# Kernel tuning notes

Hardware: AMD Instinct MI355X
Metric: run time of the kernel (lower is better)

## Reference

```python
import jax, jax.numpy as jnp
import numpy as np

N = 100000
E = 1600000
F_DIM = 128
HEADS = 8
C = F_DIM // HEADS  # 16
NEG_SLOPE = 0.2
EPS = 1e-5


def setup_inputs() -> dict:
    key = jax.random.key(0)
    ks = jax.random.split(key, 12)
    s = 1.0 / np.sqrt(F_DIM)
    x = jax.random.normal(ks[0], (N, F_DIM), dtype=jnp.float32)
    edge_index = jax.random.randint(ks[1], (2, E), 0, N, dtype=jnp.int32)
    edge_attr = jax.random.uniform(ks[2], (E, 1), dtype=jnp.float32)
    W_src = jax.random.normal(ks[3], (F_DIM, HEADS * C), dtype=jnp.float32) * s
    b_src = jnp.zeros((HEADS * C,), dtype=jnp.float32)
    W_dst = jax.random.normal(ks[4], (F_DIM, HEADS * C), dtype=jnp.float32) * s
    b_dst = jnp.zeros((HEADS * C,), dtype=jnp.float32)
    W_edge = jax.random.normal(ks[5], (1, HEADS * C), dtype=jnp.float32)
    att = jax.random.normal(ks[6], (HEADS, C), dtype=jnp.float32) * (1.0 / np.sqrt(C))
    bias = jnp.zeros((HEADS * C,), dtype=jnp.float32)
    gamma = jnp.ones((F_DIM,), dtype=jnp.float32)
    beta = jnp.zeros((F_DIM,), dtype=jnp.float32)
    return {"x": x, "edge_index": edge_index, "edge_attr": edge_attr,
            "W_src": W_src, "b_src": b_src, "W_dst": W_dst, "b_dst": b_dst,
            "W_edge": W_edge, "att": att, "bias": bias,
            "gamma": gamma, "beta": beta}


def _gatv2_block(x, edge_index, edge_attr, W_src, b_src, W_dst, b_dst, W_edge, att, bias, gamma, beta):
    src = edge_index[0]  # message sources j
    dst = edge_index[1]  # message targets i
    # linear projections, per-head view [N, H, C]
    x_src = (x @ W_src + b_src).reshape(N, HEADS, C)
    x_dst = (x @ W_dst + b_dst).reshape(N, HEADS, C)
    e_emb = (edge_attr @ W_edge).reshape(E, HEADS, C)
    # GATv2 edge scores: a^T LeakyReLU(x_i + x_j + e_ij)
    msg_src = x_src[src]                                   # [E, H, C]
    h = jax.nn.leaky_relu(msg_src + x_dst[dst] + e_emb, NEG_SLOPE)
    logits = jnp.einsum('ehc,hc->eh', h, att)              # [E, H]
    # segment softmax over incoming edges of each target node
    m = jax.ops.segment_max(logits, dst, num_segments=N)   # [N, H]
    m = jnp.where(jnp.isfinite(m), m, 0.0)
    ex = jnp.exp(logits - m[dst])
    denom = jax.ops.segment_sum(ex, dst, num_segments=N)   # [N, H]
    alpha = ex / (denom[dst] + 1e-16)                      # [E, H]
    # weighted aggregation (dropout disabled: eval mode)
    out = jax.ops.segment_sum(alpha[:, :, None] * msg_src, dst, num_segments=N)
    out = out.reshape(N, HEADS * C) + bias
    # LayerNorm over feature dim
    mu = jnp.mean(out, axis=-1, keepdims=True)
    var = jnp.var(out, axis=-1, keepdims=True)
    out = (out - mu) * jax.lax.rsqrt(var + EPS) * gamma + beta
    out = jax.nn.elu(out)
    return out + x  # residual


def reference(x, edge_index, edge_attr, W_src, b_src, W_dst, b_dst, W_edge, att, bias, gamma, beta):
    return _gatv2_block(x, edge_index, edge_attr, W_src, b_src, W_dst, b_dst, W_edge, att, bias, gamma, beta)
```

## Files before the change

### kernel.cpp

```cpp
#include <hip/hip_runtime.h>
#include <hip/hip_fp16.h>

#define NN 100000
#define EE 1600000
#define CAP 64
#define NEG_SLOPE 0.2f
#define NEG_INF (-1e30f)

#define NPART 196
#define PSHIFT 9
#define CAPP 10240
#define EPB 4096
#define P1_BLOCKS 391

struct alignas(8) H4 { __half2 a, b; };
struct alignas(16) H8 { __half2 a, b, c, d; };

using f16x8 = __attribute__((ext_vector_type(8))) _Float16;
using f32x4 = __attribute__((ext_vector_type(4))) float;

__global__ __launch_bounds__(512) void partition_kernel(
    const int* __restrict__ ei, const float* __restrict__ eattr,
    int* __restrict__ partCount, uint2* __restrict__ partBuf) {
  __shared__ int hist[NPART];
  __shared__ int base[NPART];
  for (int i = threadIdx.x; i < NPART; i += 512) hist[i] = 0;
  __syncthreads();
  const int e0 = blockIdx.x * EPB;
  int p[8], rank[8];
  uint2 rec[8];
#pragma unroll
  for (int j = 0; j < 8; ++j) {
    const int e = e0 + j * 512 + threadIdx.x;
    if (e < EE) {
      const int dst = ei[EE + e];
      const int src = ei[e];
      const unsigned q = (unsigned)__float2uint_rn(eattr[e] * 32767.0f);
      p[j] = dst >> PSHIFT;
      rec[j].x = (unsigned)(dst & 511);
      rec[j].y = (q << 17) | (unsigned)src;
      rank[j] = atomicAdd(&hist[p[j]], 1);
    } else {
      p[j] = -1;
    }
  }
  __syncthreads();
  for (int i = threadIdx.x; i < NPART; i += 512)
    base[i] = atomicAdd(&partCount[i], hist[i]);
  __syncthreads();
#pragma unroll
  for (int j = 0; j < 8; ++j) {
    if (p[j] >= 0) {
      const int idx = base[p[j]] + rank[j];
      if (idx < CAPP) partBuf[(size_t)p[j] * CAPP + idx] = rec[j];
    }
  }
}

__global__ __launch_bounds__(512) void bucket2_kernel(
    const int* __restrict__ partCount, const uint2* __restrict__ partBuf,
    int* __restrict__ counts, unsigned* __restrict__ buckets) {
  __shared__ int cnt[512];
  const int pbase = blockIdx.x << PSHIFT;
  cnt[threadIdx.x] = 0;
  __syncthreads();
  int n = partCount[blockIdx.x];
  if (n > CAPP) n = CAPP;
  for (int i = threadIdx.x; i < n; i += 512) {
    const uint2 r = partBuf[(size_t)blockIdx.x * CAPP + i];
    const int pos = atomicAdd(&cnt[r.x], 1);
    if (pos < CAP) buckets[((size_t)(pbase + (int)r.x) << 6) + pos] = r.y;
  }
  __syncthreads();
  const int node = pbase + threadIdx.x;
  if (node < NN) counts[node] = cnt[threadIdx.x];
}

__global__ __launch_bounds__(512) void proj_mfma(const float* __restrict__ x,
                                                 const float* __restrict__ Wsrc,
                                                 const float* __restrict__ bsrc,
                                                 const float* __restrict__ Wdst,
                                                 const float* __restrict__ bdst,
                                                 __half* __restrict__ xsrc,
                                                 float* __restrict__ xdst) {
  const int lane = threadIdx.x & 63;
  const int nc = threadIdx.x >> 6;
  const int r = lane & 15;
  const int kg = lane >> 4;
  const int col = nc * 16 + r;

  f16x8 bs[4], bd[4];
#pragma unroll
  for (int kk = 0; kk < 4; ++kk) {
    const int kbase = kk * 32 + kg * 8;
#pragma unroll
    for (int j = 0; j < 8; ++j) {
      bs[kk][j] = (_Float16)Wsrc[(size_t)(kbase + j) * 128 + col];
      bd[kk][j] = (_Float16)Wdst[(size_t)(kbase + j) * 128 + col];
    }
  }
  const float bsv = bsrc[col];
  const float bdv = bdst[col];

  for (int t = blockIdx.x; t < NN / 16; t += gridDim.x) {
    const int r0 = t * 16;
    f16x8 a[4];
#pragma unroll
    for (int kk = 0; kk < 4; ++kk) {
      const float* xp = x + (size_t)(r0 + r) * 128 + kk * 32 + kg * 8;
      const float4 lo = *(const float4*)xp;
      const float4 hi = *(const float4*)(xp + 4);
      a[kk][0] = (_Float16)lo.x; a[kk][1] = (_Float16)lo.y;
      a[kk][2] = (_Float16)lo.z; a[kk][3] = (_Float16)lo.w;
      a[kk][4] = (_Float16)hi.x; a[kk][5] = (_Float16)hi.y;
      a[kk][6] = (_Float16)hi.z; a[kk][7] = (_Float16)hi.w;
    }
    f32x4 accs = {bsv, bsv, bsv, bsv};
    f32x4 accd = {bdv, bdv, bdv, bdv};
#pragma unroll
    for (int kk = 0; kk < 4; ++kk) {
      accs = __builtin_amdgcn_mfma_f32_16x16x32_f16(a[kk], bs[kk], accs, 0, 0, 0);
      accd = __builtin_amdgcn_mfma_f32_16x16x32_f16(a[kk], bd[kk], accd, 0, 0, 0);
    }
#pragma unroll
    for (int reg = 0; reg < 4; ++reg) {
      const size_t row = r0 + kg * 4 + reg;
      xsrc[row * 128 + col] = __float2half(accs[reg]);
      xdst[row * 128 + col] = accd[reg];
    }
  }
}

__global__ __launch_bounds__(256) void node_kernel(
    const __half* __restrict__ xsrc, const float* __restrict__ xdst,
    const int* __restrict__ counts, const unsigned* __restrict__ buckets,
    const float* __restrict__ Wedge, const float* __restrict__ att,
    const float* __restrict__ bias, const float* __restrict__ gamma,
    const float* __restrict__ beta, const float* __restrict__ x,
    float* __restrict__ out) {
  const int lane = threadIdx.x & 63;
  const int node = blockIdx.x * 4 + (threadIdx.x >> 6);
  const int g = lane >> 4;
  const int sl = lane & 15;
  const int c0 = sl * 8;

  int deg = __builtin_nontemporal_load(&counts[node]);
  if (deg > CAP) deg = CAP;

  unsigned rec_l = 0;
  if (lane < deg) rec_l = __builtin_nontemporal_load(&buckets[node * CAP + lane]);

  const float4 xdA = *(const float4*)(xdst + (size_t)node * 128 + c0);
  const float4 xdB = *(const float4*)(xdst + (size_t)node * 128 + c0 + 4);
  const float4 weA = *(const float4*)(Wedge + c0);
  const float4 weB = *(const float4*)(Wedge + c0 + 4);
  const float4 atA = *(const float4*)(att + c0);
  const float4 atB = *(const float4*)(att + c0 + 4);

  float m = NEG_INF, den = 0.f;
  float4 accA = {0.f, 0.f, 0.f, 0.f};
  float4 accB = {0.f, 0.f, 0.f, 0.f};

#define PREFA(kk, V, EA, HV)                               \
  {                                                        \
    const int idx = (kk) + g;                              \
    V = idx < deg;                                         \
    const int ii = V ? idx : dlast;                        \
    const unsigned rec = __shfl((int)rec_l, ii);           \
    EA = (float)(rec >> 17) * (1.f / 32767.f);             \
    const int s = rec & 0x1FFFF;                           \
    HV = ((const H8*)(xsrc + (size_t)s * 128))[sl];        \
  }

#define COMPUTE(V, EA, HV)                                         \
  {                                                                \
    const float2 f0 = __half22float2(HV.a);                        \
    const float2 f1 = __half22float2(HV.b);                        \
    const float2 f2 = __half22float2(HV.c);                        \
    const float2 f3 = __half22float2(HV.d);                        \
    const float4 VA = {f0.x, f0.y, f1.x, f1.y};                    \
    const float4 VB = {f2.x, f2.y, f3.x, f3.y};                    \
    float t, lr, p = 0.f;                                          \
    t = VA.x + xdA.x + EA * weA.x; lr = fmaxf(t, NEG_SLOPE * t); p = fmaf(lr, atA.x, p); \
    t = VA.y + xdA.y + EA * weA.y; lr = fmaxf(t, NEG_SLOPE * t); p = fmaf(lr, atA.y, p); \
    t = VA.z + xdA.z + EA * weA.z; lr = fmaxf(t, NEG_SLOPE * t); p = fmaf(lr, atA.z, p); \
    t = VA.w + xdA.w + EA * weA.w; lr = fmaxf(t, NEG_SLOPE * t); p = fmaf(lr, atA.w, p); \
    t = VB.x + xdB.x + EA * weB.x; lr = fmaxf(t, NEG_SLOPE * t); p = fmaf(lr, atB.x, p); \
    t = VB.y + xdB.y + EA * weB.y; lr = fmaxf(t, NEG_SLOPE * t); p = fmaf(lr, atB.y, p); \
    t = VB.z + xdB.z + EA * weB.z; lr = fmaxf(t, NEG_SLOPE * t); p = fmaf(lr, atB.z, p); \
    t = VB.w + xdB.w + EA * weB.w; lr = fmaxf(t, NEG_SLOPE * t); p = fmaf(lr, atB.w, p); \
    p += __shfl_xor(p, 1);                                         \
    p = V ? p : NEG_INF;                                           \
    if (p <= m) {                       \
      float ex = V ? __expf(p - m) : 0.f;                          \
      den += ex;                                                   \
      accA.x = fmaf(ex, VA.x, accA.x); accA.y = fmaf(ex, VA.y, accA.y); \
      accA.z = fmaf(ex, VA.z, accA.z); accA.w = fmaf(ex, VA.w, accA.w); \
      accB.x = fmaf(ex, VB.x, accB.x); accB.y = fmaf(ex, VB.y, accB.y); \
      accB.z = fmaf(ex, VB.z, accB.z); accB.w = fmaf(ex, VB.w, accB.w); \
    } else {                                  \
      const float sc = __expf(m - p);                              \
      den = fmaf(den, sc, 1.f);                                    \
      accA.x = fmaf(accA.x, sc, VA.x); accA.y = fmaf(accA.y, sc, VA.y); \
      accA.z = fmaf(accA.z, sc, VA.z); accA.w = fmaf(accA.w, sc, VA.w); \
      accB.x = fmaf(accB.x, sc, VB.x); accB.y = fmaf(accB.y, sc, VB.y); \
      accB.z = fmaf(accB.z, sc, VB.z); accB.w = fmaf(accB.w, sc, VB.w); \
      m = p;                                                       \
    }                                                              \
  }

  if (deg > 0) {
    const int dlast = deg - 1;
    bool v0, v1, v2, v3;
    float e0, e1, e2, e3;
    H8 h0, h1, h2, h3;
    PREFA(0, v0, e0, h0);
    PREFA(4, v1, e1, h1);
    PREFA(8, v2, e2, h2);
    PREFA(12, v3, e3, h3);
    for (int k = 0; k < deg; k += 4) {
      COMPUTE(v0, e0, h0);
      v0 = v1; e0 = e1; h0 = h1;
      v1 = v2; e1 = e2; h1 = h2;
      v2 = v3; e2 = e3; h2 = h3;
      PREFA(k + 16, v3, e3, h3);
    }
  }
#undef PREFA
#undef COMPUTE

#pragma unroll
  for (int d = 16; d < 64; d <<= 1) {
    const float mo = __shfl_xor(m, d);
    const float dno = __shfl_xor(den, d);
    const float oAx = __shfl_xor(accA.x, d), oAy = __shfl_xor(accA.y, d);
    const float oAz = __shfl_xor(accA.z, d), oAw = __shfl_xor(accA.w, d);
    const float oBx = __shfl_xor(accB.x, d), oBy = __shfl_xor(accB.y, d);
    const float oBz = __shfl_xor(accB.z, d), oBw = __shfl_xor(accB.w, d);
    const float mn = fmaxf(m, mo);
    const float sa = __expf(m - mn);
    const float sb = __expf(mo - mn);
    den = den * sa + dno * sb;
    accA.x = accA.x * sa + oAx * sb; accA.y = accA.y * sa + oAy * sb;
    accA.z = accA.z * sa + oAz * sb; accA.w = accA.w * sa + oAw * sb;
    accB.x = accB.x * sa + oBx * sb; accB.y = accB.y * sa + oBy * sb;
    accB.z = accB.z * sa + oBz * sb; accB.w = accB.w * sa + oBw * sb;
    m = mn;
  }

  const float inv = den > 0.f ? 1.f / den : 0.f;
  float o[8];
  const float4 biA = *(const float4*)(bias + c0);
  const float4 biB = *(const float4*)(bias + c0 + 4);
  o[0] = accA.x * inv + biA.x; o[1] = accA.y * inv + biA.y;
  o[2] = accA.z * inv + biA.z; o[3] = accA.w * inv + biA.w;
  o[4] = accB.x * inv + biB.x; o[5] = accB.y * inv + biB.y;
  o[6] = accB.z * inv + biB.z; o[7] = accB.w * inv + biB.w;

  float s = 0.f;
#pragma unroll
  for (int j = 0; j < 8; ++j) s += o[j];
#pragma unroll
  for (int d = 1; d < 16; d <<= 1) s += __shfl_xor(s, d);
  const float mu = s * (1.f / 128.f);
  float q = 0.f;
#pragma unroll
  for (int j = 0; j < 8; ++j) {
    o[j] -= mu;
    q += o[j] * o[j];
  }
#pragma unroll
  for (int d = 1; d < 16; d <<= 1) q += __shfl_xor(q, d);
  const float r = rsqrtf(q * (1.f / 128.f) + 1e-5f);

  if (g == 0) {
    const float4 gaA = *(const float4*)(gamma + c0);
    const float4 gaB = *(const float4*)(gamma + c0 + 4);
    const float4 beA = *(const float4*)(beta + c0);
    const float4 beB = *(const float4*)(beta + c0 + 4);
    const float4 xrA = *(const float4*)(x + (size_t)node * 128 + c0);
    const float4 xrB = *(const float4*)(x + (size_t)node * 128 + c0 + 4);
    float ga[8] = {gaA.x, gaA.y, gaA.z, gaA.w, gaB.x, gaB.y, gaB.z, gaB.w};
    float be[8] = {beA.x, beA.y, beA.z, beA.w, beB.x, beB.y, beB.z, beB.w};
    float xr[8] = {xrA.x, xrA.y, xrA.z, xrA.w, xrB.x, xrB.y, xrB.z, xrB.w};
    float y[8];
#pragma unroll
    for (int j = 0; j < 8; ++j) {
      float v = o[j] * r * ga[j] + be[j];
      v = v > 0.f ? v : expm1f(v);
      y[j] = v + xr[j];
    }
    float4 oA = {y[0], y[1], y[2], y[3]};
    float4 oB = {y[4], y[5], y[6], y[7]};
    *(float4*)(out + (size_t)node * 128 + c0) = oA;
    *(float4*)(out + (size_t)node * 128 + c0 + 4) = oB;
  }
}

extern "C" void kernel_launch(void* const* d_in, const int* in_sizes, int n_in,
                              void* d_out, int out_size, void* d_ws, size_t ws_size,
                              hipStream_t stream) {
  const float* x = (const float*)d_in[0];
  const int* ei = (const int*)d_in[1];
  const float* eattr = (const float*)d_in[2];
  const float* Wsrc = (const float*)d_in[3];
  const float* bsrc = (const float*)d_in[4];
  const float* Wdst = (const float*)d_in[5];
  const float* bdst = (const float*)d_in[6];
  const float* Wedge = (const float*)d_in[7];
  const float* att = (const float*)d_in[8];
  const float* bias = (const float*)d_in[9];
  const float* gamma = (const float*)d_in[10];
  const float* beta = (const float*)d_in[11];
  float* out = (float*)d_out;

  __half* xsrc = (__half*)d_ws;
  float* xdst = (float*)(xsrc + (size_t)NN * 128);
  int* counts = (int*)(xdst + (size_t)NN * 128);
  unsigned* buckets = (unsigned*)(counts + NN);
  int* partCount = (int*)(buckets + (size_t)NN * CAP);
  uint2* partBuf = (uint2*)(partCount + 256);

  hipMemsetAsync(partCount, 0, NPART * sizeof(int), stream);
  partition_kernel<<<dim3(P1_BLOCKS), dim3(512), 0, stream>>>(ei, eattr, partCount, partBuf);
  bucket2_kernel<<<dim3(NPART), dim3(512), 0, stream>>>(partCount, partBuf, counts, buckets);
  proj_mfma<<<dim3(512), dim3(512), 0, stream>>>(x, Wsrc, bsrc, Wdst, bdst, xsrc, xdst);
  node_kernel<<<dim3(NN / 4), dim3(256), 0, stream>>>(xsrc, xdst, counts, buckets,
                                                      Wedge, att, bias, gamma,
                                                      beta, x, out);
}
```

Before: 209.4 us.

## Merge partition and projection kernels into one launch and store xdst in fp16

The edge partition kernel and the MFMA projection kernel become one launch whose block range is split: the first blocks partition edges and the rest compute projections, so the two independent stages run concurrently and one launch is removed. The x_dst projection is now stored as fp16 instead of fp32, which halves its write and read traffic and lets node_kernel load it as a single 16-byte vector. The trade-off is reduced precision for x_dst and uneven work across the merged grid.

```diff
diff --git a/kernel.cpp b/kernel.cpp
--- a/kernel.cpp
+++ b/kernel.cpp
@@ -12,6 +12,7 @@
 #define CAPP 10240
 #define EPB 4096
 #define P1_BLOCKS 391
+#define PROJ_BLOCKS 512
 
 struct alignas(8) H4 { __half2 a, b; };
 struct alignas(16) H8 { __half2 a, b, c, d; };
@@ -19,40 +20,105 @@
 using f16x8 = __attribute__((ext_vector_type(8))) _Float16;
 using f32x4 = __attribute__((ext_vector_type(4))) float;
 
-__global__ __launch_bounds__(512) void partition_kernel(
+__device__ __forceinline__ float4 h4tof4lo(const H8& h) {
+  const float2 a = __half22float2(h.a);
+  const float2 b = __half22float2(h.b);
+  return make_float4(a.x, a.y, b.x, b.y);
+}
+__device__ __forceinline__ float4 h4tof4hi(const H8& h) {
+  const float2 a = __half22float2(h.c);
+  const float2 b = __half22float2(h.d);
+  return make_float4(a.x, a.y, b.x, b.y);
+}
+
+__global__ __launch_bounds__(512) void part_proj(
     const int* __restrict__ ei, const float* __restrict__ eattr,
-    int* __restrict__ partCount, uint2* __restrict__ partBuf) {
+    int* __restrict__ partCount, uint2* __restrict__ partBuf,
+    const float* __restrict__ x, const float* __restrict__ Wsrc,
+    const float* __restrict__ bsrc, const float* __restrict__ Wdst,
+    const float* __restrict__ bdst, __half* __restrict__ xsrc,
+    __half* __restrict__ xdst) {
   __shared__ int hist[NPART];
   __shared__ int base[NPART];
-  for (int i = threadIdx.x; i < NPART; i += 512) hist[i] = 0;
-  __syncthreads();
-  const int e0 = blockIdx.x * EPB;
-  int p[8], rank[8];
-  uint2 rec[8];
-#pragma unroll
-  for (int j = 0; j < 8; ++j) {
-    const int e = e0 + j * 512 + threadIdx.x;
-    if (e < EE) {
-      const int dst = ei[EE + e];
-      const int src = ei[e];
-      const unsigned q = (unsigned)__float2uint_rn(eattr[e] * 32767.0f);
-      p[j] = dst >> PSHIFT;
-      rec[j].x = (unsigned)(dst & 511);
-      rec[j].y = (q << 17) | (unsigned)src;
-      rank[j] = atomicAdd(&hist[p[j]], 1);
-    } else {
-      p[j] = -1;
-    }
-  }
-  __syncthreads();
-  for (int i = threadIdx.x; i < NPART; i += 512)
-    base[i] = atomicAdd(&partCount[i], hist[i]);
-  __syncthreads();
-#pragma unroll
-  for (int j = 0; j < 8; ++j) {
-    if (p[j] >= 0) {
-      const int idx = base[p[j]] + rank[j];
-      if (idx < CAPP) partBuf[(size_t)p[j] * CAPP + idx] = rec[j];
+  if (blockIdx.x < P1_BLOCKS) {
+    for (int i = threadIdx.x; i < NPART; i += 512) hist[i] = 0;
+    __syncthreads();
+    const int e0 = blockIdx.x * EPB;
+    int p[8], rank[8];
+    uint2 rec[8];
+#pragma unroll
+    for (int j = 0; j < 8; ++j) {
+      const int e = e0 + j * 512 + threadIdx.x;
+      if (e < EE) {
+        const int dst = ei[EE + e];
+        const int src = ei[e];
+        const unsigned q = (unsigned)__float2uint_rn(eattr[e] * 32767.0f);
+        p[j] = dst >> PSHIFT;
+        rec[j].x = (unsigned)(dst & 511);
+        rec[j].y = (q << 17) | (unsigned)src;
+        rank[j] = atomicAdd(&hist[p[j]], 1);
+      } else {
+        p[j] = -1;
+      }
+    }
+    __syncthreads();
+    for (int i = threadIdx.x; i < NPART; i += 512)
+      base[i] = atomicAdd(&partCount[i], hist[i]);
+    __syncthreads();
+#pragma unroll
+    for (int j = 0; j < 8; ++j) {
+      if (p[j] >= 0) {
+        const int idx = base[p[j]] + rank[j];
+        if (idx < CAPP) partBuf[(size_t)p[j] * CAPP + idx] = rec[j];
+      }
+    }
+    return;
+  }
+  const int bid = blockIdx.x - P1_BLOCKS;
+  const int lane = threadIdx.x & 63;
+  const int nc = threadIdx.x >> 6;
+  const int r = lane & 15;
+  const int kg = lane >> 4;
+  const int col = nc * 16 + r;
+
+  f16x8 bs[4], bd[4];
+#pragma unroll
+  for (int kk = 0; kk < 4; ++kk) {
+    const int kbase = kk * 32 + kg * 8;
+#pragma unroll
+    for (int j = 0; j < 8; ++j) {
+      bs[kk][j] = (_Float16)Wsrc[(size_t)(kbase + j) * 128 + col];
+      bd[kk][j] = (_Float16)Wdst[(size_t)(kbase + j) * 128 + col];
+    }
+  }
+  const float bsv = bsrc[col];
+  const float bdv = bdst[col];
+
+  for (int t = bid; t < NN / 16; t += PROJ_BLOCKS) {
+    const int r0 = t * 16;
+    f16x8 a[4];
+#pragma unroll
+    for (int kk = 0; kk < 4; ++kk) {
+      const float* xp = x + (size_t)(r0 + r) * 128 + kk * 32 + kg * 8;
+      const float4 lo = *(const float4*)xp;
+      const float4 hi = *(const float4*)(xp + 4);
+      a[kk][0] = (_Float16)lo.x; a[kk][1] = (_Float16)lo.y;
+      a[kk][2] = (_Float16)lo.z; a[kk][3] = (_Float16)lo.w;
+      a[kk][4] = (_Float16)hi.x; a[kk][5] = (_Float16)hi.y;
+      a[kk][6] = (_Float16)hi.z; a[kk][7] = (_Float16)hi.w;
+    }
+    f32x4 accs = {bsv, bsv, bsv, bsv};
+    f32x4 accd = {bdv, bdv, bdv, bdv};
+#pragma unroll
+    for (int kk = 0; kk < 4; ++kk) {
+      accs = __builtin_amdgcn_mfma_f32_16x16x32_f16(a[kk], bs[kk], accs, 0, 0, 0);
+      accd = __builtin_amdgcn_mfma_f32_16x16x32_f16(a[kk], bd[kk], accd, 0, 0, 0);
+    }
+#pragma unroll
+    for (int reg = 0; reg < 4; ++reg) {
+      const size_t row = r0 + kg * 4 + reg;
+      xsrc[row * 128 + col] = __float2half(accs[reg]);
+      xdst[row * 128 + col] = __float2half(accd[reg]);
     }
   }
 }
@@ -76,63 +142,8 @@
   if (node < NN) counts[node] = cnt[threadIdx.x];
 }
 
-__global__ __launch_bounds__(512) void proj_mfma(const float* __restrict__ x,
-                                                 const float* __restrict__ Wsrc,
-                                                 const float* __restrict__ bsrc,
-                                                 const float* __restrict__ Wdst,
-                                                 const float* __restrict__ bdst,
-                                                 __half* __restrict__ xsrc,
-                                                 float* __restrict__ xdst) {
-  const int lane = threadIdx.x & 63;
-  const int nc = threadIdx.x >> 6;
-  const int r = lane & 15;
-  const int kg = lane >> 4;
-  const int col = nc * 16 + r;
-
-  f16x8 bs[4], bd[4];
-#pragma unroll
-  for (int kk = 0; kk < 4; ++kk) {
-    const int kbase = kk * 32 + kg * 8;
-#pragma unroll
-    for (int j = 0; j < 8; ++j) {
-      bs[kk][j] = (_Float16)Wsrc[(size_t)(kbase + j) * 128 + col];
-      bd[kk][j] = (_Float16)Wdst[(size_t)(kbase + j) * 128 + col];
-    }
-  }
-  const float bsv = bsrc[col];
-  const float bdv = bdst[col];
-
-  for (int t = blockIdx.x; t < NN / 16; t += gridDim.x) {
-    const int r0 = t * 16;
-    f16x8 a[4];
-#pragma unroll
-    for (int kk = 0; kk < 4; ++kk) {
-      const float* xp = x + (size_t)(r0 + r) * 128 + kk * 32 + kg * 8;
-      const float4 lo = *(const float4*)xp;
-      const float4 hi = *(const float4*)(xp + 4);
-      a[kk][0] = (_Float16)lo.x; a[kk][1] = (_Float16)lo.y;
-      a[kk][2] = (_Float16)lo.z; a[kk][3] = (_Float16)lo.w;
-      a[kk][4] = (_Float16)hi.x; a[kk][5] = (_Float16)hi.y;
-      a[kk][6] = (_Float16)hi.z; a[kk][7] = (_Float16)hi.w;
-    }
-    f32x4 accs = {bsv, bsv, bsv, bsv};
-    f32x4 accd = {bdv, bdv, bdv, bdv};
-#pragma unroll
-    for (int kk = 0; kk < 4; ++kk) {
-      accs = __builtin_amdgcn_mfma_f32_16x16x32_f16(a[kk], bs[kk], accs, 0, 0, 0);
-      accd = __builtin_amdgcn_mfma_f32_16x16x32_f16(a[kk], bd[kk], accd, 0, 0, 0);
-    }
-#pragma unroll
-    for (int reg = 0; reg < 4; ++reg) {
-      const size_t row = r0 + kg * 4 + reg;
-      xsrc[row * 128 + col] = __float2half(accs[reg]);
-      xdst[row * 128 + col] = accd[reg];
-    }
-  }
-}
-
 __global__ __launch_bounds__(256) void node_kernel(
-    const __half* __restrict__ xsrc, const float* __restrict__ xdst,
+    const __half* __restrict__ xsrc, const __half* __restrict__ xdst,
     const int* __restrict__ counts, const unsigned* __restrict__ buckets,
     const float* __restrict__ Wedge, const float* __restrict__ att,
     const float* __restrict__ bias, const float* __restrict__ gamma,
@@ -150,8 +161,9 @@
   unsigned rec_l = 0;
   if (lane < deg) rec_l = __builtin_nontemporal_load(&buckets[node * CAP + lane]);
 
-  const float4 xdA = *(const float4*)(xdst + (size_t)node * 128 + c0);
-  const float4 xdB = *(const float4*)(xdst + (size_t)node * 128 + c0 + 4);
+  const H8 xdh = ((const H8*)(xdst + (size_t)node * 128))[sl];
+  const float4 xdA = h4tof4lo(xdh);
+  const float4 xdB = h4tof4hi(xdh);
   const float4 weA = *(const float4*)(Wedge + c0);
   const float4 weB = *(const float4*)(Wedge + c0 + 4);
   const float4 atA = *(const float4*)(att + c0);
@@ -174,12 +186,8 @@
 
 #define COMPUTE(V, EA, HV)                                         \
   {                                                                \
-    const float2 f0 = __half22float2(HV.a);                        \
-    const float2 f1 = __half22float2(HV.b);                        \
-    const float2 f2 = __half22float2(HV.c);                        \
-    const float2 f3 = __half22float2(HV.d);                        \
-    const float4 VA = {f0.x, f0.y, f1.x, f1.y};                    \
-    const float4 VB = {f2.x, f2.y, f3.x, f3.y};                    \
+    const float4 VA = h4tof4lo(HV);                                \
+    const float4 VB = h4tof4hi(HV);                                \
     float t, lr, p = 0.f;                                          \
     t = VA.x + xdA.x + EA * weA.x; lr = fmaxf(t, NEG_SLOPE * t); p = fmaf(lr, atA.x, p); \
     t = VA.y + xdA.y + EA * weA.y; lr = fmaxf(t, NEG_SLOPE * t); p = fmaf(lr, atA.y, p); \
@@ -315,16 +323,16 @@
   float* out = (float*)d_out;
 
   __half* xsrc = (__half*)d_ws;
-  float* xdst = (float*)(xsrc + (size_t)NN * 128);
+  __half* xdst = xsrc + (size_t)NN * 128;
   int* counts = (int*)(xdst + (size_t)NN * 128);
   unsigned* buckets = (unsigned*)(counts + NN);
   int* partCount = (int*)(buckets + (size_t)NN * CAP);
   uint2* partBuf = (uint2*)(partCount + 256);
 
   hipMemsetAsync(partCount, 0, NPART * sizeof(int), stream);
-  partition_kernel<<<dim3(P1_BLOCKS), dim3(512), 0, stream>>>(ei, eattr, partCount, partBuf);
+  part_proj<<<dim3(P1_BLOCKS + PROJ_BLOCKS), dim3(512), 0, stream>>>(
+      ei, eattr, partCount, partBuf, x, Wsrc, bsrc, Wdst, bdst, xsrc, xdst);
   bucket2_kernel<<<dim3(NPART), dim3(512), 0, stream>>>(partCount, partBuf, counts, buckets);
-  proj_mfma<<<dim3(512), dim3(512), 0, stream>>>(x, Wsrc, bsrc, Wdst, bdst, xsrc, xdst);
   node_kernel<<<dim3(NN / 4), dim3(256), 0, stream>>>(xsrc, xdst, counts, buckets,
                                                       Wedge, att, bias, gamma,
                                                       beta, x, out);
```

Result: slower. 221.5 us (+5.8%).
